# Optimization experiments

Measured on AMD Instinct MI355X. Metric: run time of the kernel, lower is better.

## Reference

```python
import jax, jax.numpy as jnp
import numpy as np

BASE_TEMP = 0.07
CLASS_TEMPS = jnp.array([0.08, 0.05, 0.10], dtype=jnp.float32)  # idx 0,1,2
EPS = 1e-08


def setup_inputs() -> dict:
    key = jax.random.key(0)
    k1, k2 = jax.random.split(key)
    B, D = 8192, 128
    embeddings = jax.random.normal(k1, (B, D), dtype=jnp.float32)
    labels = jax.random.randint(k2, (B,), 0, 3, dtype=jnp.int64)
    return {"embeddings": embeddings, "labels": labels}


def reference(embeddings, labels):
    B = embeddings.shape[0]
    # per-row temperature from the row's class label
    temps = CLASS_TEMPS[labels]  # [B]
    sim = jnp.matmul(embeddings, embeddings.T)  # [B, B]
    logits = sim / temps[:, None]
    # subtract detached row max (stability, gradient-stopped as in .detach())
    logits = logits - jax.lax.stop_gradient(jnp.max(logits, axis=1, keepdims=True))
    # denominator includes the self term (original sums exp over all j)
    log_prob = logits - jnp.log(jnp.sum(jnp.exp(logits), axis=1, keepdims=True) + EPS)
    # positives: same label, excluding self
    pos_mask = (labels[:, None] == labels[None, :]).astype(jnp.float32)
    pos_mask = pos_mask * (1.0 - jnp.eye(B, dtype=jnp.float32))
    pos_count = jnp.sum(pos_mask, axis=1)  # [B]
    valid = pos_count > 0
    loss_i = -(BASE_TEMP / temps) * jnp.sum(pos_mask * log_prob, axis=1) / (pos_count + EPS)
    n_valid = jnp.sum(valid.astype(jnp.float32))
    total = jnp.sum(jnp.where(valid, loss_i, 0.0))
    return jnp.where(n_valid > 0, total / jnp.maximum(n_valid, 1.0), 0.0)
```

## Files before the change

kernel.cpp:

```cpp
#include <hip/hip_runtime.h>
#include <hip/hip_bf16.h>


#define B_ROWS 8192
#define D_DIM 128
#define NSPLIT 16
#define JRANGE (B_ROWS / NSPLIT)
#define NSTEPS (JRANGE / 32)
#define BASE_TEMP 0.07f
#define LOG2E 1.4426950408889634f
#define LN2 0.6931471805599453f
#define FIX_SCALE 1048576.0f

typedef __bf16 bf16x8 __attribute__((ext_vector_type(8)));
typedef __bf16 bf16x4 __attribute__((ext_vector_type(4)));
typedef float floatx16 __attribute__((ext_vector_type(16)));
typedef unsigned long long u64;

__device__ __forceinline__ float class_invtemp(int lbl) {
    return (lbl == 0) ? 12.5f : ((lbl == 1) ? 20.0f : 10.0f);
}

__device__ __forceinline__ u64 fix64(float v) {
    return (u64)(long long)llrintf(v * FIX_SCALE);
}

__global__ __launch_bounds__(256) void kz_zero(u64* __restrict__ a) {
    a[threadIdx.x] = 0ull;
    a[256 + threadIdx.x] = 0ull;
}

__global__ __launch_bounds__(256) void k0_prep(
        const float* __restrict__ E, const int* __restrict__ labels,
        __bf16* __restrict__ Ebf, __bf16* __restrict__ Ebs,
        float* __restrict__ nrm,
        u64* __restrict__ Sfix , u64* __restrict__ cntfix ) {
    const int blk = blockIdx.x;
    const int tid = threadIdx.x;
    const int row0 = blk * 32;

    __shared__ float sh[3][128];
    __shared__ int scnt[3];
    if (tid < 3) scnt[tid] = 0;

    const float4* src = reinterpret_cast<const float4*>(E + (size_t)row0 * D_DIM);
    #pragma unroll
    for (int p = 0; p < 4; ++p) {
        int idx = p * 256 + tid;
        float4 v = src[idx];
        int r = idx >> 5, k4 = idx & 31;
        int R = row0 + r;
        float sc = class_invtemp(labels[R]) * LOG2E;
        int T = R >> 5;
        int l = (R & 31) + ((k4 >> 1) & 1) * 32;
        int c = k4 >> 2;
        size_t dst = (size_t)T * 4096 + c * 512 + l * 8 + (k4 & 1) * 4;
        bf16x4 o  = { (__bf16)v.x, (__bf16)v.y, (__bf16)v.z, (__bf16)v.w };
        bf16x4 os = { (__bf16)(v.x * sc), (__bf16)(v.y * sc),
                      (__bf16)(v.z * sc), (__bf16)(v.w * sc) };
        *reinterpret_cast<bf16x4*>(Ebf + dst) = o;
        *reinterpret_cast<bf16x4*>(Ebs + dst) = os;
        float s = v.x * v.x + v.y * v.y + v.z * v.z + v.w * v.w;
        s += __shfl_xor(s, 1);  s += __shfl_xor(s, 2);  s += __shfl_xor(s, 4);
        s += __shfl_xor(s, 8);  s += __shfl_xor(s, 16);
        if ((tid & 31) == 0) nrm[R] = s;
    }

    const int d = tid & 127, half = tid >> 7;
    float s0 = 0.f, s1 = 0.f, s2 = 0.f;
    #pragma unroll 4
    for (int r2 = 0; r2 < 16; ++r2) {
        int r = row0 + half * 16 + r2;
        float v = E[(size_t)r * D_DIM + d];
        int l = labels[r];
        s0 += (l == 0) ? v : 0.f;
        s1 += (l == 1) ? v : 0.f;
        s2 += (l == 2) ? v : 0.f;
    }
    if (half == 1) { sh[0][d] = s0; sh[1][d] = s1; sh[2][d] = s2; }
    if (tid < 32) atomicAdd(&scnt[labels[row0 + tid]], 1);
    __syncthreads();
    if (half == 0) {
        atomicAdd(&Sfix[d],       fix64(s0 + sh[0][d]));
        atomicAdd(&Sfix[128 + d], fix64(s1 + sh[1][d]));
        atomicAdd(&Sfix[256 + d], fix64(s2 + sh[2][d]));
    }
    __syncthreads();
    if (tid < 3) atomicAdd(&cntfix[tid], (u64)scnt[tid]);
}

__global__ __launch_bounds__(256) void k2_stats(
        const __bf16* __restrict__ Ebf, const __bf16* __restrict__ Ebs,
        const int* __restrict__ labels, const float* __restrict__ nrm,
        float* __restrict__ part ) {
    const int tid = threadIdx.x;
    const int lane = tid & 63;
    const int wave = tid >> 6;
    const int itile = blockIdx.x;
    const int split = blockIdx.y;
    const int col = lane & 31;
    const int icol0 = itile * 256 + wave * 64 + col;
    const int icol1 = icol0 + 32;

    const float bs0 = class_invtemp(labels[icol0]) * LOG2E;
    const float bs1 = class_invtemp(labels[icol1]) * LOG2E;
    const float negm0 = -bs0 * nrm[icol0];
    const float negm1 = -bs1 * nrm[icol1];

    const int iT0 = itile * 8 + wave * 2;
    const __bf16* b0 = Ebs + (size_t)iT0 * 4096 + lane * 8;
    const __bf16* b1 = b0 + 4096;
    bf16x8 Bf0[8], Bf1[8];
    #pragma unroll
    for (int c = 0; c < 8; ++c) {
        Bf0[c] = *reinterpret_cast<const bf16x8*>(b0 + c * 512);
        Bf1[c] = *reinterpret_cast<const bf16x8*>(b1 + c * 512);
    }

    const __bf16* abase = Ebf + (size_t)split * NSTEPS * 4096 + lane * 8;
    bf16x8 A0[8], A1[8];
    #pragma unroll
    for (int c = 0; c < 8; ++c)
        A0[c] = *reinterpret_cast<const bf16x8*>(abase + c * 512);

    float Zacc0[4], Zacc1[4];
    #pragma unroll
    for (int q = 0; q < 4; ++q) { Zacc0[q] = 0.f; Zacc1[q] = 0.f; }

    auto k2_step = [&](const bf16x8* Ab) {
        floatx16 a0, a1;
        #pragma unroll
        for (int r = 0; r < 16; ++r) { a0[r] = negm0; a1[r] = negm1; }
        #pragma unroll
        for (int c = 0; c < 8; ++c) {
            a0 = __builtin_amdgcn_mfma_f32_32x32x16_bf16(Ab[c], Bf0[c], a0, 0, 0, 0);
            a1 = __builtin_amdgcn_mfma_f32_32x32x16_bf16(Ab[c], Bf1[c], a1, 0, 0, 0);
        }
        #pragma unroll
        for (int q = 0; q < 4; ++q) {
            Zacc0[q] += (__builtin_amdgcn_exp2f(a0[4 * q])
                       + __builtin_amdgcn_exp2f(a0[4 * q + 1]))
                      + (__builtin_amdgcn_exp2f(a0[4 * q + 2])
                       + __builtin_amdgcn_exp2f(a0[4 * q + 3]));
            Zacc1[q] += (__builtin_amdgcn_exp2f(a1[4 * q])
                       + __builtin_amdgcn_exp2f(a1[4 * q + 1]))
                      + (__builtin_amdgcn_exp2f(a1[4 * q + 2])
                       + __builtin_amdgcn_exp2f(a1[4 * q + 3]));
        }
    };

    for (int s = 0; s < NSTEPS; s += 2) {
        {
            const __bf16* ap = abase + (size_t)(s + 1) * 4096;
            #pragma unroll
            for (int c = 0; c < 8; ++c)
                A1[c] = *reinterpret_cast<const bf16x8*>(ap + c * 512);
            k2_step(A0);
        }
        {
            if (s + 2 < NSTEPS) {
                const __bf16* ap = abase + (size_t)(s + 2) * 4096;
                #pragma unroll
                for (int c = 0; c < 8; ++c)
                    A0[c] = *reinterpret_cast<const bf16x8*>(ap + c * 512);
            }
            k2_step(A1);
        }
    }

    float Zt0 = (Zacc0[0] + Zacc0[1]) + (Zacc0[2] + Zacc0[3]);
    float Zt1 = (Zacc1[0] + Zacc1[1]) + (Zacc1[2] + Zacc1[3]);
    Zt0 += __shfl_xor(Zt0, 32);
    Zt1 += __shfl_xor(Zt1, 32);
    if (lane < 32) {
        part[(size_t)split * B_ROWS + icol0] = Zt0;
        part[(size_t)split * B_ROWS + icol1] = Zt1;
    }
}

__global__ __launch_bounds__(256) void k3_rowloss(
        const float* __restrict__ E, const int* __restrict__ labels,
        const u64* __restrict__ Sfix, const u64* __restrict__ cntfix,
        const float* __restrict__ nrm, const float* __restrict__ part,
        u64* __restrict__ lossfix, u64* __restrict__ validfix,
        unsigned int* __restrict__ done, float* __restrict__ out) {
    __shared__ float sS[384];
    const int tid = threadIdx.x;
    if (tid < 128) {
        sS[tid]       = (float)(long long)Sfix[tid]       * (1.0f / FIX_SCALE);
        sS[128 + tid] = (float)(long long)Sfix[128 + tid] * (1.0f / FIX_SCALE);
        sS[256 + tid] = (float)(long long)Sfix[256 + tid] * (1.0f / FIX_SCALE);
    }
    __syncthreads();

    const int r = tid >> 3, g = tid & 7;
    const int i = blockIdx.x * 32 + r;
    const int lab = labels[i];
    const float invt = class_invtemp(lab);

    const float4* er = reinterpret_cast<const float4*>(E + (size_t)i * D_DIM);
    const float4* sr = reinterpret_cast<const float4*>(&sS[lab * 128]);
    float dotS = 0.f;
    #pragma unroll
    for (int q = 0; q < 4; ++q) {
        float4 v = er[g * 4 + q];
        float4 s = sr[g * 4 + q];
        dotS += v.x * s.x + v.y * s.y + v.z * s.z + v.w * s.w;
    }
    float Zp = 0.f;
    #pragma unroll
    for (int p = 0; p < NSPLIT / 8; ++p)
        Zp += part[(size_t)(g + p * 8) * B_ROWS + i];

    #pragma unroll
    for (int off = 1; off < 8; off <<= 1) {
        dotS += __shfl_xor(dotS, off);
        Zp   += __shfl_xor(Zp, off);
    }

    float loss = 0.f;
    int valid = 0;
    if (g == 0) {
        const float nr = nrm[i];
        const float C = (float)(long long)cntfix[lab] - 1.0f;
        const float lse = invt * nr + LN2 * __builtin_amdgcn_logf(Zp);
        const float P_nat = invt * (dotS - nr);
        if (C > 0.f) {
            loss = -(BASE_TEMP * invt) * (P_nat - C * lse) / (C + 1e-8f);
            valid = 1;
        }
    }
    loss += __shfl_down(loss, 8);   valid += __shfl_down(valid, 8);
    loss += __shfl_down(loss, 16);  valid += __shfl_down(valid, 16);
    loss += __shfl_down(loss, 32);  valid += __shfl_down(valid, 32);

    __shared__ float rl[4];
    __shared__ int rv[4];
    if ((tid & 63) == 0) { rl[tid >> 6] = loss; rv[tid >> 6] = valid; }
    __syncthreads();
    if (tid == 0) {
        float bt = (rl[0] + rl[1]) + (rl[2] + rl[3]);
        int bv = (rv[0] + rv[1]) + (rv[2] + rv[3]);
        atomicAdd(lossfix, fix64(bt));
        atomicAdd(validfix, (u64)bv);
        __threadfence();
        unsigned int t = atomicAdd(done, 1u);
        if (t == gridDim.x - 1) {
            u64 L = atomicAdd(lossfix, 0ull);
            u64 V = atomicAdd(validfix, 0ull);
            double T = (double)(long long)L * (1.0 / (double)FIX_SCALE);
            double N = (double)(long long)V;
            out[0] = (N > 0.0) ? (float)(T / fmax(N, 1.0)) : 0.f;
        }
    }
}

extern "C" void kernel_launch(void* const* d_in, const int* in_sizes, int n_in,
                              void* d_out, int out_size, void* d_ws, size_t ws_size,
                              hipStream_t stream) {
    const float* E = (const float*)d_in[0];
    const int* labels = (const int*)d_in[1];
    float* out = (float*)d_out;
    char* ws = (char*)d_ws;

    const size_t OFF_EBF  = 0;
    const size_t OFF_EBS  = (size_t)2 << 20;
    const size_t OFF_ATOM = (size_t)4 << 20;
    const size_t OFF_NRM  = OFF_ATOM + 4096;
    const size_t OFF_PART = OFF_NRM + (size_t)B_ROWS * 4;

    __bf16* Ebf = (__bf16*)(ws + OFF_EBF);
    __bf16* Ebs = (__bf16*)(ws + OFF_EBS);
    u64* Sfix = (u64*)(ws + OFF_ATOM);
    u64* cntfix = Sfix + 384;
    u64* lossfix = Sfix + 388;
    u64* validfix = Sfix + 389;
    unsigned int* done = (unsigned int*)(Sfix + 390);
    float* nrm = (float*)(ws + OFF_NRM);
    float* part = (float*)(ws + OFF_PART);

    kz_zero<<<1, 256, 0, stream>>>(Sfix);
    k0_prep<<<256, 256, 0, stream>>>(E, labels, Ebf, Ebs, nrm, Sfix, cntfix);
    k2_stats<<<dim3(32, NSPLIT), 256, 0, stream>>>(Ebf, Ebs, labels, nrm, part);
    k3_rowloss<<<256, 256, 0, stream>>>(E, labels, Sfix, cntfix, nrm, part,
                                        lossfix, validfix, done, out);
}
```

Baseline: 49.05 us.

## Drop zero kernel, replace fixed-point atomics with partials, stage A tiles in LDS

After: 48.46 us. About the same (-1.2%).

```diff
diff --git a/kernel.cpp b/kernel.cpp
--- a/kernel.cpp
+++ b/kernel.cpp
@@ -25,16 +25,12 @@
     return (u64)(long long)llrintf(v * FIX_SCALE);
 }
 
-__global__ __launch_bounds__(256) void kz_zero(u64* __restrict__ a) {
-    a[threadIdx.x] = 0ull;
-    a[256 + threadIdx.x] = 0ull;
-}
-
 __global__ __launch_bounds__(256) void k0_prep(
         const float* __restrict__ E, const int* __restrict__ labels,
         __bf16* __restrict__ Ebf, __bf16* __restrict__ Ebs,
         float* __restrict__ nrm,
-        u64* __restrict__ Sfix , u64* __restrict__ cntfix ) {
+        float* __restrict__ Spart ,
+        int* __restrict__ cntpart ) {
     const int blk = blockIdx.x;
     const int tid = threadIdx.x;
     const int row0 = blk * 32;
@@ -81,18 +77,23 @@
     if (tid < 32) atomicAdd(&scnt[labels[row0 + tid]], 1);
     __syncthreads();
     if (half == 0) {
-        atomicAdd(&Sfix[d],       fix64(s0 + sh[0][d]));
-        atomicAdd(&Sfix[128 + d], fix64(s1 + sh[1][d]));
-        atomicAdd(&Sfix[256 + d], fix64(s2 + sh[2][d]));
-    }
-    __syncthreads();
-    if (tid < 3) atomicAdd(&cntfix[tid], (u64)scnt[tid]);
-}
-
-__global__ __launch_bounds__(256) void k2_stats(
+        Spart[((size_t)blk * 3 + 0) * 128 + d] = s0 + sh[0][d];
+        Spart[((size_t)blk * 3 + 1) * 128 + d] = s1 + sh[1][d];
+        Spart[((size_t)blk * 3 + 2) * 128 + d] = s2 + sh[2][d];
+    }
+    if (tid < 3) cntpart[blk * 4 + tid] = scnt[tid];
+}
+
+__global__ __launch_bounds__(256, 2) void k2_stats(
         const __bf16* __restrict__ Ebf, const __bf16* __restrict__ Ebs,
         const int* __restrict__ labels, const float* __restrict__ nrm,
-        float* __restrict__ part ) {
+        float* __restrict__ part ,
+        const float* __restrict__ Spart, const int* __restrict__ cntpart,
+        float* __restrict__ S , float* __restrict__ counts ,
+        u64* __restrict__ lossfix, u64* __restrict__ validfix,
+        unsigned int* __restrict__ done) {
+    __shared__ __bf16 Ab[2][4096];
+
     const int tid = threadIdx.x;
     const int lane = tid & 63;
     const int wave = tid >> 6;
@@ -102,40 +103,56 @@
     const int icol0 = itile * 256 + wave * 64 + col;
     const int icol1 = icol0 + 32;
 
-    const float bs0 = class_invtemp(labels[icol0]) * LOG2E;
-    const float bs1 = class_invtemp(labels[icol1]) * LOG2E;
-    const float negm0 = -bs0 * nrm[icol0];
-    const float negm1 = -bs1 * nrm[icol1];
+    const float negm0 = -class_invtemp(labels[icol0]) * LOG2E * nrm[icol0];
+    const float negm1 = -class_invtemp(labels[icol1]) * LOG2E * nrm[icol1];
 
     const int iT0 = itile * 8 + wave * 2;
     const __bf16* b0 = Ebs + (size_t)iT0 * 4096 + lane * 8;
-    const __bf16* b1 = b0 + 4096;
     bf16x8 Bf0[8], Bf1[8];
     #pragma unroll
     for (int c = 0; c < 8; ++c) {
         Bf0[c] = *reinterpret_cast<const bf16x8*>(b0 + c * 512);
-        Bf1[c] = *reinterpret_cast<const bf16x8*>(b1 + c * 512);
-    }
-
-    const __bf16* abase = Ebf + (size_t)split * NSTEPS * 4096 + lane * 8;
-    bf16x8 A0[8], A1[8];
-    #pragma unroll
-    for (int c = 0; c < 8; ++c)
-        A0[c] = *reinterpret_cast<const bf16x8*>(abase + c * 512);
+        Bf1[c] = *reinterpret_cast<const bf16x8*>(b0 + 4096 + c * 512);
+    }
+
+    const __bf16* abase = Ebf + (size_t)split * NSTEPS * 4096;
+
+    {
+        const float4* s0 = reinterpret_cast<const float4*>(abase);
+        float4* d0 = reinterpret_cast<float4*>(&Ab[0][0]);
+        d0[tid] = s0[tid];
+        d0[tid + 256] = s0[tid + 256];
+    }
+    __syncthreads();
 
     float Zacc0[4], Zacc1[4];
     #pragma unroll
     for (int q = 0; q < 4; ++q) { Zacc0[q] = 0.f; Zacc1[q] = 0.f; }
 
-    auto k2_step = [&](const bf16x8* Ab) {
+    for (int s = 0; s < NSTEPS; ++s) {
+        float4 nxt0, nxt1;
+        if (s + 1 < NSTEPS) {
+            const float4* sp = reinterpret_cast<const float4*>(
+                abase + (size_t)(s + 1) * 4096);
+            nxt0 = sp[tid];
+            nxt1 = sp[tid + 256];
+        }
+
+        const __bf16* abuf = &Ab[s & 1][0];
+        bf16x8 A[8];
+        #pragma unroll
+        for (int c = 0; c < 8; ++c)
+            A[c] = *reinterpret_cast<const bf16x8*>(abuf + c * 512 + lane * 8);
+
         floatx16 a0, a1;
         #pragma unroll
         for (int r = 0; r < 16; ++r) { a0[r] = negm0; a1[r] = negm1; }
         #pragma unroll
         for (int c = 0; c < 8; ++c) {
-            a0 = __builtin_amdgcn_mfma_f32_32x32x16_bf16(Ab[c], Bf0[c], a0, 0, 0, 0);
-            a1 = __builtin_amdgcn_mfma_f32_32x32x16_bf16(Ab[c], Bf1[c], a1, 0, 0, 0);
-        }
+            a0 = __builtin_amdgcn_mfma_f32_32x32x16_bf16(A[c], Bf0[c], a0, 0, 0, 0);
+            a1 = __builtin_amdgcn_mfma_f32_32x32x16_bf16(A[c], Bf1[c], a1, 0, 0, 0);
+        }
+
         #pragma unroll
         for (int q = 0; q < 4; ++q) {
             Zacc0[q] += (__builtin_amdgcn_exp2f(a0[4 * q])
@@ -147,25 +164,13 @@
                       + (__builtin_amdgcn_exp2f(a1[4 * q + 2])
                        + __builtin_amdgcn_exp2f(a1[4 * q + 3]));
         }
-    };
-
-    for (int s = 0; s < NSTEPS; s += 2) {
-        {
-            const __bf16* ap = abase + (size_t)(s + 1) * 4096;
-            #pragma unroll
-            for (int c = 0; c < 8; ++c)
-                A1[c] = *reinterpret_cast<const bf16x8*>(ap + c * 512);
-            k2_step(A0);
-        }
-        {
-            if (s + 2 < NSTEPS) {
-                const __bf16* ap = abase + (size_t)(s + 2) * 4096;
-                #pragma unroll
-                for (int c = 0; c < 8; ++c)
-                    A0[c] = *reinterpret_cast<const bf16x8*>(ap + c * 512);
-            }
-            k2_step(A1);
-        }
+
+        if (s + 1 < NSTEPS) {
+            float4* dn = reinterpret_cast<float4*>(&Ab[(s + 1) & 1][0]);
+            dn[tid] = nxt0;
+            dn[tid + 256] = nxt1;
+        }
+        __syncthreads();
     }
 
     float Zt0 = (Zacc0[0] + Zacc0[1]) + (Zacc0[2] + Zacc0[3]);
@@ -176,20 +181,39 @@
         part[(size_t)split * B_ROWS + icol0] = Zt0;
         part[(size_t)split * B_ROWS + icol1] = Zt1;
     }
+
+    if (split == 0) {
+        if (itile < 3 && tid < 128) {
+            float a = 0.f;
+            #pragma unroll 8
+            for (int g = 0; g < 256; ++g)
+                a += Spart[((size_t)g * 3 + itile) * 128 + tid];
+            S[itile * 128 + tid] = a;
+        } else if (itile == 3 && tid < 3) {
+            int a = 0;
+            #pragma unroll 8
+            for (int g = 0; g < 256; ++g) a += cntpart[g * 4 + tid];
+            counts[tid] = (float)a;
+        } else if (itile == 4 && tid == 0) {
+            *lossfix = 0ull;
+            *validfix = 0ull;
+            *done = 0u;
+        }
+    }
 }
 
 __global__ __launch_bounds__(256) void k3_rowloss(
         const float* __restrict__ E, const int* __restrict__ labels,
-        const u64* __restrict__ Sfix, const u64* __restrict__ cntfix,
+        const float* __restrict__ S, const float* __restrict__ counts,
         const float* __restrict__ nrm, const float* __restrict__ part,
         u64* __restrict__ lossfix, u64* __restrict__ validfix,
         unsigned int* __restrict__ done, float* __restrict__ out) {
     __shared__ float sS[384];
     const int tid = threadIdx.x;
     if (tid < 128) {
-        sS[tid]       = (float)(long long)Sfix[tid]       * (1.0f / FIX_SCALE);
-        sS[128 + tid] = (float)(long long)Sfix[128 + tid] * (1.0f / FIX_SCALE);
-        sS[256 + tid] = (float)(long long)Sfix[256 + tid] * (1.0f / FIX_SCALE);
+        sS[tid]       = S[tid];
+        sS[128 + tid] = S[128 + tid];
+        sS[256 + tid] = S[256 + tid];
     }
     __syncthreads();
 
@@ -222,7 +246,7 @@
     int valid = 0;
     if (g == 0) {
         const float nr = nrm[i];
-        const float C = (float)(long long)cntfix[lab] - 1.0f;
+        const float C = counts[lab] - 1.0f;
         const float lse = invt * nr + LN2 * __builtin_amdgcn_logf(Zp);
         const float P_nat = invt * (dotS - nr);
         if (C > 0.f) {
@@ -263,25 +287,31 @@
     float* out = (float*)d_out;
     char* ws = (char*)d_ws;
 
-    const size_t OFF_EBF  = 0;
-    const size_t OFF_EBS  = (size_t)2 << 20;
-    const size_t OFF_ATOM = (size_t)4 << 20;
-    const size_t OFF_NRM  = OFF_ATOM + 4096;
-    const size_t OFF_PART = OFF_NRM + (size_t)B_ROWS * 4;
+    const size_t OFF_EBF   = 0;
+    const size_t OFF_EBS   = (size_t)2 << 20;
+    const size_t OFF_NRM   = (size_t)4 << 20;
+    const size_t OFF_SPART = OFF_NRM + 32768;
+    const size_t OFF_CNTP  = OFF_SPART + 393216;
+    const size_t OFF_S     = OFF_CNTP + 4096;
+    const size_t OFF_MISC  = OFF_S + 2048;
+    const size_t OFF_PART  = OFF_MISC + 256;
 
     __bf16* Ebf = (__bf16*)(ws + OFF_EBF);
     __bf16* Ebs = (__bf16*)(ws + OFF_EBS);
-    u64* Sfix = (u64*)(ws + OFF_ATOM);
-    u64* cntfix = Sfix + 384;
-    u64* lossfix = Sfix + 388;
-    u64* validfix = Sfix + 389;
-    unsigned int* done = (unsigned int*)(Sfix + 390);
     float* nrm = (float*)(ws + OFF_NRM);
+    float* Spart = (float*)(ws + OFF_SPART);
+    int* cntpart = (int*)(ws + OFF_CNTP);
+    float* S = (float*)(ws + OFF_S);
+    float* counts = (float*)(ws + OFF_MISC);
+    u64* lossfix = (u64*)(ws + OFF_MISC + 16);
+    u64* validfix = (u64*)(ws + OFF_MISC + 24);
+    unsigned int* done = (unsigned int*)(ws + OFF_MISC + 32);
     float* part = (float*)(ws + OFF_PART);
 
-    kz_zero<<<1, 256, 0, stream>>>(Sfix);
-    k0_prep<<<256, 256, 0, stream>>>(E, labels, Ebf, Ebs, nrm, Sfix, cntfix);
-    k2_stats<<<dim3(32, NSPLIT), 256, 0, stream>>>(Ebf, Ebs, labels, nrm, part);
-    k3_rowloss<<<256, 256, 0, stream>>>(E, labels, Sfix, cntfix, nrm, part,
+    k0_prep<<<256, 256, 0, stream>>>(E, labels, Ebf, Ebs, nrm, Spart, cntpart);
+    k2_stats<<<dim3(32, NSPLIT), 256, 0, stream>>>(
+        Ebf, Ebs, labels, nrm, part, Spart, cntpart, S, counts,
+        lossfix, validfix, done);
+    k3_rowloss<<<256, 256, 0, stream>>>(E, labels, S, counts, nrm, part,
                                         lossfix, validfix, done, out);
 }
```
